# Kernel optimization log

Hardware: AMD Instinct MI355X
Metric: run time of the kernel (lower is better)

Reference implementation:

```python
import jax, jax.numpy as jnp
import numpy as np

N_NODES = 100000
N_EDGES = 6400000
F_IN = 128
F_OUT = 16


def setup_inputs() -> dict:
    key = jax.random.key(0)
    k1, k2, k3 = jax.random.split(key, 3)
    x = jax.random.normal(k1, (N_NODES, F_IN), dtype=jnp.float32)
    edge_index = jax.random.randint(k2, (2, N_EDGES), 0, N_NODES, dtype=jnp.int64)
    W = jax.random.normal(k3, (F_IN, F_OUT), dtype=jnp.float32) / np.sqrt(F_IN)
    b = jnp.zeros((F_OUT,), dtype=jnp.float32)
    return {"x": x, "edge_index": edge_index, "W": W, "b": b}


def reference(x, edge_index, W, b):
    # GCNConv (PyG defaults: add self-loops, symmetric normalization) -> tanh -> mean pool
    N = x.shape[0]
    loops = jnp.arange(N, dtype=edge_index.dtype)
    row = jnp.concatenate([edge_index[0], loops])  # source nodes
    col = jnp.concatenate([edge_index[1], loops])  # target nodes
    # degree of target nodes (edge weight 1.0)
    deg = jax.ops.segment_sum(jnp.ones(row.shape[0], dtype=x.dtype), col, num_segments=N)
    dinv = jnp.where(deg > 0, jax.lax.rsqrt(deg), 0.0)
    norm = dinv[row] * dinv[col]  # [E+N]
    h = x @ W  # [N, F_OUT] transform first (cheaper than transforming messages)
    msgs = h[row] * norm[:, None]  # gather + scale
    out = jax.ops.segment_sum(msgs, col, num_segments=N) + b  # scatter-add
    h = jnp.tanh(out)
    # MeanAggregation over all nodes -> single graph embedding [1, F_OUT]
    return jnp.mean(h, axis=0, keepdims=True)
```

## Files before the change

### kernel.cpp

```cpp
#include <hip/hip_runtime.h>
#include <math.h>

#define N_NODES 100000
#define N_EDGES 6400000
#define F_IN 128
#define F_OUT 16
#define NB 391
#define NBLK 1600
#define EPB 4000
#define LOCW 392
#define KPB 3
#define ACCN (NB * 256 * F_OUT)
#define QSCALE 1024.0f
#define QINV   (1.0f / 1024.0f)

__global__ void __launch_bounds__(256) count_kernel(const int* __restrict__ col,
                                                    int* __restrict__ loc) {
    __shared__ int hist[NB];
    const int t = threadIdx.x, k = blockIdx.x;
    for (int i = t; i < NB; i += 256) hist[i] = 0;
    __syncthreads();
    const int e0 = k * EPB;
    for (int i = t; i < EPB; i += 256) atomicAdd(&hist[col[e0 + i] >> 8], 1);
    __syncthreads();
    for (int b = t; b < NB; b += 256) loc[k * LOCW + b] = hist[b];
}

__global__ void __launch_bounds__(256) desta_kernel(const int* __restrict__ loc,
        int* __restrict__ destT, int* __restrict__ total) {
    __shared__ int tsum[256];
    const int t = threadIdx.x, b = blockIdx.x;
    int v[7]; int s = 0;
    #pragma unroll
    for (int j = 0; j < 7; j++) {
        int k = t * 7 + j;
        v[j] = (k < NBLK) ? loc[k * LOCW + b] : 0;
        s += v[j];
    }
    tsum[t] = s;
    __syncthreads();
    for (int off = 1; off < 256; off <<= 1) {
        int a = (t >= off) ? tsum[t - off] : 0;
        __syncthreads();
        tsum[t] += a;
        __syncthreads();
    }
    int run = tsum[t] - s;
    #pragma unroll
    for (int j = 0; j < 7; j++) {
        int k = t * 7 + j;
        if (k < NBLK) destT[(size_t)b * NBLK + k] = run;
        run += v[j];
    }
    if (t == 255) total[b] = tsum[255];
}

__global__ void destb_kernel(const int* __restrict__ total, int* __restrict__ boffs) {
    __shared__ int lds[512];
    const int t = threadIdx.x;
    int v = (t < NB) ? total[t] : 0;
    lds[t] = v; __syncthreads();
    for (int off = 1; off < 512; off <<= 1) {
        int a = (t >= off) ? lds[t - off] : 0; __syncthreads();
        lds[t] += a; __syncthreads();
    }
    if (t < NB) boffs[t] = lds[t] - v;
    if (t == NB) boffs[NB] = N_EDGES;
}

__global__ void __launch_bounds__(256) place_kernel(const int* __restrict__ row,
        const int* __restrict__ col, const int* __restrict__ destT,
        const int* __restrict__ boffs, unsigned int* __restrict__ packed) {
    __shared__ int hist[NB];
    __shared__ int scanb[512];
    __shared__ int base[NB];
    __shared__ int gadj[NB];
    __shared__ unsigned int tile[EPB];
    __shared__ unsigned short tileb[EPB];
    const int t = threadIdx.x, k = blockIdx.x;
    const int e0 = k * EPB;
    int myc[16], myr[16];
    #pragma unroll
    for (int j = 0; j < 16; j++) {
        int idx = t + j * 256;
        if (idx < EPB) { myc[j] = col[e0 + idx]; myr[j] = row[e0 + idx]; }
        else { myc[j] = -1; myr[j] = 0; }
    }
    for (int i = t; i < NB; i += 256) hist[i] = 0;
    __syncthreads();
    #pragma unroll
    for (int j = 0; j < 16; j++)
        if (myc[j] >= 0) atomicAdd(&hist[myc[j] >> 8], 1);
    __syncthreads();
    scanb[t] = (t < NB) ? hist[t] : 0;
    scanb[t + 256] = (t + 256 < NB) ? hist[t + 256] : 0;
    __syncthreads();
    for (int off = 1; off < 512; off <<= 1) {
        int a  = (t >= off) ? scanb[t - off] : 0;
        int a2 = scanb[t + 256 - off];
        __syncthreads();
        scanb[t] += a; scanb[t + 256] += a2;
        __syncthreads();
    }
    if (t < NB) base[t] = scanb[t] - hist[t];
    if (t + 256 < NB) base[t + 256] = scanb[t + 256] - hist[t + 256];
    __syncthreads();
    for (int bb = t; bb < NB; bb += 256) {
        gadj[bb] = boffs[bb] + destT[(size_t)bb * NBLK + k] - base[bb];
        hist[bb] = 0;
    }
    __syncthreads();
    #pragma unroll
    for (int j = 0; j < 16; j++) {
        if (myc[j] >= 0) {
            int bb = myc[j] >> 8;
            int pos = base[bb] + atomicAdd(&hist[bb], 1);
            tile[pos] = ((unsigned)myr[j] << 8) | (unsigned)(myc[j] & 255);
            tileb[pos] = (unsigned short)bb;
        }
    }
    __syncthreads();
    for (int i = t; i < EPB; i += 256)
        packed[gadj[tileb[i]] + i] = tile[i];
}

__global__ void __launch_bounds__(256) deg_kernel(const unsigned int* __restrict__ packed,
        const int* __restrict__ boffs, float* __restrict__ dinv) {
    __shared__ int dh[256];
    const int t = threadIdx.x, b = blockIdx.x;
    dh[t] = 0;
    __syncthreads();
    const int e = boffs[b + 1];
    for (int i = boffs[b] + t; i < e; i += 256)
        atomicAdd(&dh[packed[i] & 255u], 1);
    __syncthreads();
    const int node = (b << 8) + t;
    if (node < N_NODES) dinv[node] = rsqrtf((float)dh[t] + 1.0f);
}

__global__ void gemm_kernel(const float* __restrict__ x, const float* __restrict__ W,
                            const float* __restrict__ dinv, short* __restrict__ gq) {
    __shared__ float Ws[F_IN * F_OUT];
    __shared__ float xs[16 * (F_IN + 1)];
    const int tid = threadIdx.x;
    const int n0 = blockIdx.x * 16;
    for (int i = tid; i < F_IN * F_OUT; i += 256) Ws[i] = W[i];
    const float* xbase = x + (size_t)n0 * F_IN;
    for (int i = tid; i < 16 * F_IN; i += 256) {
        int r = i >> 7, c = i & 127;
        xs[r * (F_IN + 1) + c] = xbase[i];
    }
    __syncthreads();
    const int node = tid >> 4, f = tid & 15;
    const float* xr = &xs[node * (F_IN + 1)];
    float acc = 0.f;
    #pragma unroll 8
    for (int k = 0; k < F_IN; k++) acc += xr[k] * Ws[k * 16 + f];
    float v = acc * dinv[n0 + node] * QSCALE;
    v = fminf(fmaxf(v, -32000.f), 32000.f);
    gq[n0 * 16 + tid] = (short)__float2int_rn(v);
}

__global__ void __launch_bounds__(256) scatter_kernel(
        const unsigned int* __restrict__ packed, const int* __restrict__ boffs,
        const short* __restrict__ gq, int* __restrict__ accp) {
    __shared__ int sacc[256 * F_OUT];
    const int t = threadIdx.x;
    for (int i = t; i < 256 * F_OUT; i += 256) sacc[i] = 0;
    __syncthreads();
    const int b = blockIdx.x, part = blockIdx.y;
    const int s = boffs[b], e = boffs[b + 1];
    const int chunk = (e - s + KPB - 1) / KPB;
    const int cs = s + part * chunk;
    const int ce = min(cs + chunk, e);
    const int f = t & 15, eg = t >> 4;
    int i = cs + eg;
    for (; i + 48 < ce; i += 64) {
        unsigned p0 = packed[i];
        unsigned p1 = packed[i + 16];
        unsigned p2 = packed[i + 32];
        unsigned p3 = packed[i + 48];
        int v0 = gq[(p0 >> 8) * 16 + f];
        int v1 = gq[(p1 >> 8) * 16 + f];
        int v2 = gq[(p2 >> 8) * 16 + f];
        int v3 = gq[(p3 >> 8) * 16 + f];
        atomicAdd(&sacc[((p0 & 255u) << 4) + f], v0);
        atomicAdd(&sacc[((p1 & 255u) << 4) + f], v1);
        atomicAdd(&sacc[((p2 & 255u) << 4) + f], v2);
        atomicAdd(&sacc[((p3 & 255u) << 4) + f], v3);
    }
    for (; i < ce; i += 16) {
        unsigned p0 = packed[i];
        atomicAdd(&sacc[((p0 & 255u) << 4) + f], (int)gq[(p0 >> 8) * 16 + f]);
    }
    __syncthreads();
    const int nbase = b << 8;
    int* dst = accp + (size_t)part * ACCN + ((size_t)nbase << 4);
    for (int j = t; j < 256 * F_OUT; j += 256)
        if (nbase + (j >> 4) < N_NODES) dst[j] = sacc[j];
}

__global__ void finalize_kernel(const int* __restrict__ accp, const short* __restrict__ gq,
                                const float* __restrict__ dinv, const float* __restrict__ b,
                                double* __restrict__ dsum) {
    __shared__ float s[4][16];
    const int tid = threadIdx.x;
    const int f = tid & 15;
    const float bf = b[f];
    float local = 0.f;
    for (int i = blockIdx.x * blockDim.x + tid; i < N_NODES * F_OUT;
         i += gridDim.x * blockDim.x) {
        const int n = i >> 4;
        int ai = accp[i] + accp[ACCN + i] + accp[2 * ACCN + i] + (int)gq[i];
        local += tanhf(dinv[n] * ((float)ai * QINV) + bf);
    }
    local += __shfl_down(local, 32);
    local += __shfl_down(local, 16);
    const int lane = tid & 63, wave = tid >> 6;
    if (lane < 16) s[wave][lane] = local;
    __syncthreads();
    if (tid < 16) {
        float v = s[0][tid] + s[1][tid] + s[2][tid] + s[3][tid];
        atomicAdd(&dsum[tid], (double)v);
    }
}

__global__ void out_kernel(const double* __restrict__ dsum, float* __restrict__ out) {
    const int f = threadIdx.x;
    if (f < 16) out[f] = (float)(dsum[f] * (1.0 / (double)N_NODES));
}

extern "C" void kernel_launch(void* const* d_in, const int* in_sizes, int n_in,
                              void* d_out, int out_size, void* d_ws, size_t ws_size,
                              hipStream_t stream) {
    const float* x  = (const float*)d_in[0];
    const int*   ei = (const int*)d_in[1];
    const float* W  = (const float*)d_in[2];
    const float* b  = (const float*)d_in[3];
    float* out = (float*)d_out;

    const int* row = ei;
    const int* col = ei + N_EDGES;

    char* p = (char*)d_ws;
    double*       dsum   = (double*)p;        p += 16 * 8;
    int*          loc    = (int*)p;           p += (size_t)NBLK * LOCW * 4;
    int*          destT  = (int*)p;           p += (size_t)NB * NBLK * 4;
    int*          total  = (int*)p;           p += NB * 4;
    int*          boffs  = (int*)p;           p += (NB + 1) * 4;
    float*        dinv   = (float*)p;         p += (size_t)N_NODES * 4;
    short*        gq     = (short*)p;         p += (size_t)N_NODES * F_OUT * 2;
    unsigned int* packed = (unsigned int*)p;  p += (size_t)N_EDGES * 4;
    int*          accp   = (int*)p;

    hipMemsetAsync(dsum, 0, 16 * 8, stream);

    count_kernel   <<<NBLK, 256, 0, stream>>>(col, loc);
    desta_kernel   <<<NB, 256, 0, stream>>>(loc, destT, total);
    destb_kernel   <<<1, 512, 0, stream>>>(total, boffs);
    place_kernel   <<<NBLK, 256, 0, stream>>>(row, col, destT, boffs, packed);
    deg_kernel     <<<NB, 256, 0, stream>>>(packed, boffs, dinv);
    gemm_kernel    <<<N_NODES / 16, 256, 0, stream>>>(x, W, dinv, gq);
    scatter_kernel <<<dim3(NB, KPB), 256, 0, stream>>>(packed, boffs, gq, accp);
    finalize_kernel<<<640, 256, 0, stream>>>(accp, gq, dinv, b, dsum);
    out_kernel     <<<1, 16, 0, stream>>>(dsum, out);
}
```

Measured before the change: 288.2 us.

## Split degree and scatter work across more blocks, fuse output into finalize

The degree kernel is split into 4 parts per bucket and accumulates integer degrees with global atomics. dinv is now recomputed with rsqrt in the GEMM and finalize kernels. The scatter partition count rises from 3 to 4, and the GEMM uses float4 loads with a padded shared-memory row. The out kernel is folded into finalize through a last-block counter. The workspace is compacted by aliasing loc/destT with accp. The goal is to remove launches and raise parallelism, at the cost of extra atomics and one more partial accumulator to sum in finalize.

```diff
diff --git a/kernel.cpp b/kernel.cpp
--- a/kernel.cpp
+++ b/kernel.cpp
@@ -9,15 +9,20 @@
 #define NBLK 1600
 #define EPB 4000
 #define LOCW 392
-#define KPB 3
+#define KPB 4
 #define ACCN (NB * 256 * F_OUT)
 #define QSCALE 1024.0f
 #define QINV   (1.0f / 1024.0f)
+#define FIN_GRID 640
 
 __global__ void __launch_bounds__(256) count_kernel(const int* __restrict__ col,
-                                                    int* __restrict__ loc) {
+                                                    int* __restrict__ loc,
+                                                    int* __restrict__ deg) {
     __shared__ int hist[NB];
     const int t = threadIdx.x, k = blockIdx.x;
+    const int z0 = k * 63;
+    for (int j = t; j < 63; j += 256)
+        if (z0 + j < N_NODES) deg[z0 + j] = 0;
     for (int i = t; i < NB; i += 256) hist[i] = 0;
     __syncthreads();
     const int e0 = k * EPB;
@@ -125,38 +130,45 @@
 }
 
 __global__ void __launch_bounds__(256) deg_kernel(const unsigned int* __restrict__ packed,
-        const int* __restrict__ boffs, float* __restrict__ dinv) {
+        const int* __restrict__ boffs, int* __restrict__ deg) {
     __shared__ int dh[256];
-    const int t = threadIdx.x, b = blockIdx.x;
+    const int t = threadIdx.x;
     dh[t] = 0;
     __syncthreads();
-    const int e = boffs[b + 1];
-    for (int i = boffs[b] + t; i < e; i += 256)
+    const int b = blockIdx.x, part = blockIdx.y;
+    const int s = boffs[b], e = boffs[b + 1];
+    const int chunk = (e - s + 3) >> 2;
+    const int cs = s + part * chunk;
+    const int ce = min(cs + chunk, e);
+    for (int i = cs + t; i < ce; i += 256)
         atomicAdd(&dh[packed[i] & 255u], 1);
     __syncthreads();
     const int node = (b << 8) + t;
-    if (node < N_NODES) dinv[node] = rsqrtf((float)dh[t] + 1.0f);
-}
-
-__global__ void gemm_kernel(const float* __restrict__ x, const float* __restrict__ W,
-                            const float* __restrict__ dinv, short* __restrict__ gq) {
+    if (node < N_NODES && dh[t]) atomicAdd(&deg[node], dh[t]);
+}
+
+__global__ void __launch_bounds__(256) gemm_kernel(const float* __restrict__ x,
+        const float* __restrict__ W, const int* __restrict__ deg,
+        short* __restrict__ gq) {
     __shared__ float Ws[F_IN * F_OUT];
-    __shared__ float xs[16 * (F_IN + 1)];
+    __shared__ float xs[16 * 132];
     const int tid = threadIdx.x;
     const int n0 = blockIdx.x * 16;
-    for (int i = tid; i < F_IN * F_OUT; i += 256) Ws[i] = W[i];
-    const float* xbase = x + (size_t)n0 * F_IN;
-    for (int i = tid; i < 16 * F_IN; i += 256) {
-        int r = i >> 7, c = i & 127;
-        xs[r * (F_IN + 1) + c] = xbase[i];
+    const float4* W4 = (const float4*)W;
+    for (int i = tid; i < 512; i += 256) ((float4*)Ws)[i] = W4[i];
+    const float4* x4 = (const float4*)(x + (size_t)n0 * F_IN);
+    for (int i = tid; i < 512; i += 256) {
+        int n = i >> 5, j = i & 31;
+        *(float4*)(xs + n * 132 + j * 4) = x4[i];
     }
     __syncthreads();
     const int node = tid >> 4, f = tid & 15;
-    const float* xr = &xs[node * (F_IN + 1)];
+    const float* xr = &xs[node * 132];
     float acc = 0.f;
     #pragma unroll 8
     for (int k = 0; k < F_IN; k++) acc += xr[k] * Ws[k * 16 + f];
-    float v = acc * dinv[n0 + node] * QSCALE;
+    const float dinvn = rsqrtf((float)deg[n0 + node] + 1.0f);
+    float v = acc * dinvn * QSCALE;
     v = fminf(fmaxf(v, -32000.f), 32000.f);
     gq[n0 * 16 + tid] = (short)__float2int_rn(v);
 }
@@ -200,10 +212,12 @@
         if (nbase + (j >> 4) < N_NODES) dst[j] = sacc[j];
 }
 
-__global__ void finalize_kernel(const int* __restrict__ accp, const short* __restrict__ gq,
-                                const float* __restrict__ dinv, const float* __restrict__ b,
-                                double* __restrict__ dsum) {
+__global__ void __launch_bounds__(256) finalize_kernel(const int* __restrict__ accp,
+        const short* __restrict__ gq, const int* __restrict__ deg,
+        const float* __restrict__ b, double* __restrict__ dsum,
+        int* __restrict__ done, float* __restrict__ out) {
     __shared__ float s[4][16];
+    __shared__ int lastflag;
     const int tid = threadIdx.x;
     const int f = tid & 15;
     const float bf = b[f];
@@ -211,8 +225,10 @@
     for (int i = blockIdx.x * blockDim.x + tid; i < N_NODES * F_OUT;
          i += gridDim.x * blockDim.x) {
         const int n = i >> 4;
-        int ai = accp[i] + accp[ACCN + i] + accp[2 * ACCN + i] + (int)gq[i];
-        local += tanhf(dinv[n] * ((float)ai * QINV) + bf);
+        int ai = accp[i] + accp[ACCN + i] + accp[2 * ACCN + i] + accp[3 * ACCN + i]
+               + (int)gq[i];
+        float dinvn = rsqrtf((float)deg[n] + 1.0f);
+        local += tanhf(dinvn * ((float)ai * QINV) + bf);
     }
     local += __shfl_down(local, 32);
     local += __shfl_down(local, 16);
@@ -223,11 +239,15 @@
         float v = s[0][tid] + s[1][tid] + s[2][tid] + s[3][tid];
         atomicAdd(&dsum[tid], (double)v);
     }
-}
-
-__global__ void out_kernel(const double* __restrict__ dsum, float* __restrict__ out) {
-    const int f = threadIdx.x;
-    if (f < 16) out[f] = (float)(dsum[f] * (1.0 / (double)N_NODES));
+    if (tid == 0) {
+        __threadfence();
+        lastflag = (atomicAdd(done, 1) == (int)gridDim.x - 1);
+    }
+    __syncthreads();
+    if (lastflag && tid < 16) {
+        double v = atomicAdd(&dsum[tid], 0.0);
+        out[tid] = (float)(v * (1.0 / (double)N_NODES));
+    }
 }
 
 extern "C" void kernel_launch(void* const* d_in, const int* in_sizes, int n_in,
@@ -244,24 +264,25 @@
 
     char* p = (char*)d_ws;
     double*       dsum   = (double*)p;        p += 16 * 8;
-    int*          loc    = (int*)p;           p += (size_t)NBLK * LOCW * 4;
-    int*          destT  = (int*)p;           p += (size_t)NB * NBLK * 4;
-    int*          total  = (int*)p;           p += NB * 4;
+    int*          done   = (int*)p;           p += 16;
+    int*          total  = (int*)p;           p += 1568;
     int*          boffs  = (int*)p;           p += (NB + 1) * 4;
-    float*        dinv   = (float*)p;         p += (size_t)N_NODES * 4;
+    int*          deg    = (int*)p;           p += (size_t)N_NODES * 4;
     short*        gq     = (short*)p;         p += (size_t)N_NODES * F_OUT * 2;
     unsigned int* packed = (unsigned int*)p;  p += (size_t)N_EDGES * 4;
-    int*          accp   = (int*)p;
-
-    hipMemsetAsync(dsum, 0, 16 * 8, stream);
-
-    count_kernel   <<<NBLK, 256, 0, stream>>>(col, loc);
+    char*         shared = p;
+    int*          loc    = (int*)shared;
+    int*          destT  = (int*)(shared + (size_t)NBLK * LOCW * 4);
+    int*          accp   = (int*)shared;
+
+    hipMemsetAsync(dsum, 0, 16 * 8 + 16, stream);
+
+    count_kernel   <<<NBLK, 256, 0, stream>>>(col, loc, deg);
     desta_kernel   <<<NB, 256, 0, stream>>>(loc, destT, total);
     destb_kernel   <<<1, 512, 0, stream>>>(total, boffs);
     place_kernel   <<<NBLK, 256, 0, stream>>>(row, col, destT, boffs, packed);
-    deg_kernel     <<<NB, 256, 0, stream>>>(packed, boffs, dinv);
-    gemm_kernel    <<<N_NODES / 16, 256, 0, stream>>>(x, W, dinv, gq);
+    deg_kernel     <<<dim3(NB, 4), 256, 0, stream>>>(packed, boffs, deg);
+    gemm_kernel    <<<N_NODES / 16, 256, 0, stream>>>(x, W, deg, gq);
     scatter_kernel <<<dim3(NB, KPB), 256, 0, stream>>>(packed, boffs, gq, accp);
-    finalize_kernel<<<640, 256, 0, stream>>>(accp, gq, dinv, b, dsum);
-    out_kernel     <<<1, 16, 0, stream>>>(dsum, out);
-}
+    finalize_kernel<<<FIN_GRID, 256, 0, stream>>>(accp, gq, deg, b, dsum, done, out);
+}
```

After: 264.9 us. -8.1%, faster.
